# Kernel optimization log

Hardware: AMD Instinct MI355X
Metric: run time of the kernel (lower is better)

## Reference

```python
import jax, jax.numpy as jnp
import numpy as np

N, E, H, C, NG = 50000, 800000, 4, 64, 32
HC = H * C  # 256


def setup_inputs() -> dict:
    key = jax.random.key(0)
    ks = jax.random.split(key, 32)
    f32 = jnp.float32
    def rn(k, shape, s=0.1):
        return jax.random.normal(k, shape, dtype=f32) * s
    inp = {}
    inp['x'] = jax.random.normal(ks[0], (N, 4), dtype=f32)
    inp['edge_index'] = jax.random.randint(ks[1], (2, E), 0, N, dtype=jnp.int32)
    inp['edge_attr'] = jax.random.normal(ks[2], (E, 1), dtype=f32)
    inp['batch'] = jnp.sort(jax.random.randint(ks[3], (N,), 0, NG, dtype=jnp.int32))
    # encoder
    inp['enc_w'] = rn(ks[4], (4, 64)); inp['enc_b'] = rn(ks[5], (64,))
    # GATv2 layer 1: in 64 -> H*C (lin_l source, lin_r target, lin_edge, att, bias)
    inp['g1_wl'] = rn(ks[6], (64, HC)); inp['g1_bl'] = rn(ks[7], (HC,))
    inp['g1_wr'] = rn(ks[8], (64, HC)); inp['g1_br'] = rn(ks[9], (HC,))
    inp['g1_we'] = rn(ks[10], (1, HC))
    inp['g1_att'] = rn(ks[11], (H, C))
    inp['g1_bias'] = rn(ks[12], (HC,))
    # GATv2 layer 2: in 256 -> H*C
    inp['g2_wl'] = rn(ks[13], (HC, HC)); inp['g2_bl'] = rn(ks[14], (HC,))
    inp['g2_wr'] = rn(ks[15], (HC, HC)); inp['g2_br'] = rn(ks[16], (HC,))
    inp['g2_we'] = rn(ks[17], (1, HC))
    inp['g2_att'] = rn(ks[18], (H, C))
    inp['g2_bias'] = rn(ks[19], (HC,))
    # post MLP: 256 -> 128 (LayerNorm, ReLU) -> 64 (ReLU)
    inp['p1_w'] = rn(ks[20], (HC, 128)); inp['p1_b'] = rn(ks[21], (128,))
    inp['ln_g'] = jnp.ones((128,), dtype=f32); inp['ln_b'] = jnp.zeros((128,), dtype=f32)
    inp['p2_w'] = rn(ks[22], (128, 64)); inp['p2_b'] = rn(ks[23], (64,))
    return inp


def _gatv2_layer(x, src, dst, eattr, wl, bl, wr, br, we, att, bias):
    # PyG GATv2Conv: alpha_e = att . leaky_relu(lin_l(x_src) + lin_r(x_dst) + lin_edge(e))
    n = x.shape[0]
    xl = (x @ wl + bl).reshape(n, H, C)   # source-side messages
    xr = (x @ wr + br).reshape(n, H, C)   # target-side
    e = (eattr @ we).reshape(-1, H, C)
    m = jax.nn.leaky_relu(xl[src] + xr[dst] + e, 0.2)        # [E',H,C]
    alpha = jnp.einsum('ehc,hc->eh', m, att)                  # [E',H]
    amax = jax.lax.stop_gradient(jax.ops.segment_max(alpha, dst, num_segments=n))
    ex = jnp.exp(alpha - amax[dst])
    den = jax.ops.segment_sum(ex, dst, num_segments=n)
    a = ex / den[dst]                                          # softmax per dst node
    out = jax.ops.segment_sum(a[:, :, None] * xl[src], dst, num_segments=n)
    return out.reshape(n, HC) + bias


def reference(x, edge_index, edge_attr, batch, enc_w, enc_b,
              g1_wl, g1_bl, g1_wr, g1_br, g1_we, g1_att, g1_bias,
              g2_wl, g2_bl, g2_wr, g2_br, g2_we, g2_att, g2_bias,
              p1_w, p1_b, ln_g, ln_b, p2_w, p2_b):
    n = x.shape[0]
    src0, dst0 = edge_index[0], edge_index[1]
    # PyG default add_self_loops=True with fill_value='mean' for edge_attr
    deg = jnp.maximum(jax.ops.segment_sum(jnp.ones_like(edge_attr[:, 0]), dst0, num_segments=n), 1.0)
    loop_attr = jax.ops.segment_sum(edge_attr, dst0, num_segments=n) / deg[:, None]
    idx = jnp.arange(n, dtype=src0.dtype)
    src = jnp.concatenate([src0, idx]); dst = jnp.concatenate([dst0, idx])
    eattr = jnp.concatenate([edge_attr, loop_attr], axis=0)
    h = jax.nn.relu(x @ enc_w + enc_b)
    h = jax.nn.relu(_gatv2_layer(h, src, dst, eattr, g1_wl, g1_bl, g1_wr, g1_br, g1_we, g1_att, g1_bias))
    h = jax.nn.relu(_gatv2_layer(h, src, dst, eattr, g2_wl, g2_bl, g2_wr, g2_br, g2_we, g2_att, g2_bias))
    # global mean pool over graphs
    cnt = jnp.maximum(jax.ops.segment_sum(jnp.ones((n,), h.dtype), batch, num_segments=NG), 1.0)
    g = jax.ops.segment_sum(h, batch, num_segments=NG) / cnt[:, None]
    # post MLP (dropout is identity in eval)
    z = g @ p1_w + p1_b
    mu = jnp.mean(z, axis=-1, keepdims=True)
    var = jnp.mean((z - mu) ** 2, axis=-1, keepdims=True)
    z = (z - mu) / jnp.sqrt(var + 1e-5) * ln_g + ln_b
    z = jax.nn.relu(z)
    z = jax.nn.relu(z @ p2_w + p2_b)
    return z
```

## Files before the change

### kernel.cpp

```cpp
#include <hip/hip_runtime.h>

#define CDIV(a,b) (((a)+(b)-1)/(b))

typedef __bf16 bf16_t;
typedef bf16_t bf16x8 __attribute__((ext_vector_type(8)));
typedef bf16_t bf16x4 __attribute__((ext_vector_type(4)));
typedef float floatx4 __attribute__((ext_vector_type(4)));
typedef float floatx2 __attribute__((ext_vector_type(2)));

__device__ __forceinline__ int sigma2(int p) {
    int tile = p >> 7, hh = (p >> 6) & 1, m = (p >> 2) & 15, c = p & 3;
    return tile * 128 + (hh * 4 + c) * 16 + m;
}

__device__ __forceinline__ floatx2 up2(unsigned v) {
    floatx2 r;
    r.x = __uint_as_float(v << 16);
    r.y = __uint_as_float(v & 0xffff0000u);
    return r;
}

__global__ void k_deg(const int* __restrict__ ei, const float* __restrict__ ea,
                      float* __restrict__ deg, float* __restrict__ lsum, int E) {
    int e = blockIdx.x * 256 + threadIdx.x;
    if (e >= E) return;
    int d = ei[E + e];
    atomicAdd(&deg[d], 1.0f);
    atomicAdd(&lsum[d], ea[e]);
}

__global__ void k_loopattr(float* __restrict__ lsum, const float* __restrict__ deg, int n) {
    int i = blockIdx.x * 256 + threadIdx.x;
    if (i >= n) return;
    lsum[i] = lsum[i] / fmaxf(deg[i], 1.0f);
}

__global__ void k_scanA(const float* __restrict__ deg, int* __restrict__ part, int n) {
    __shared__ int sh[256];
    int t = threadIdx.x;
    int i = blockIdx.x * 256 + t;
    int v = (i < n) ? (int)deg[i] + 1 : 0;
    sh[t] = v;
    __syncthreads();
    for (int d = 128; d > 0; d >>= 1) { if (t < d) sh[t] += sh[t + d]; __syncthreads(); }
    if (t == 0) part[blockIdx.x] = sh[0];
}
__global__ void k_scanB(int* __restrict__ part, int nb) {
    __shared__ int sh[256];
    int t = threadIdx.x;
    int v = (t < nb) ? part[t] : 0;
    sh[t] = v;
    __syncthreads();
    for (int d = 1; d < 256; d <<= 1) {
        int u = (t >= d) ? sh[t - d] : 0;
        __syncthreads();
        sh[t] += u;
        __syncthreads();
    }
    if (t < nb) part[t] = sh[t] - v;
}
__global__ void k_scanC(const float* __restrict__ deg, const int* __restrict__ part,
                        int* __restrict__ off, int n) {
    __shared__ int sh[256];
    int t = threadIdx.x;
    int i = blockIdx.x * 256 + t;
    int v = (i < n) ? (int)deg[i] + 1 : 0;
    sh[t] = v;
    __syncthreads();
    for (int d = 1; d < 256; d <<= 1) {
        int u = (t >= d) ? sh[t - d] : 0;
        __syncthreads();
        sh[t] += u;
        __syncthreads();
    }
    int excl = part[blockIdx.x] + sh[t] - v;
    if (i < n) off[i] = excl;
    if (i == n - 1) off[n] = excl + v;
}

__global__ void k_fill(const int* __restrict__ ei, const float* __restrict__ ea,
                       const float* __restrict__ lattr, const int* __restrict__ off,
                       int* __restrict__ cursor, int* __restrict__ csr_src,
                       float* __restrict__ csr_ea, int E, int n) {
    int e = blockIdx.x * 256 + threadIdx.x;
    int EE = E + n;
    if (e >= EE) return;
    int s, d; float a;
    if (e < E) { s = ei[e]; d = ei[E + e]; a = ea[e]; }
    else       { s = e - E; d = s;         a = lattr[s]; }
    int pos = off[d] + atomicAdd(&cursor[d], 1);
    csr_src[pos] = s;
    csr_ea[pos] = a;
}

__global__ void k_enc(const float* __restrict__ x, const float* __restrict__ w,
                      const float* __restrict__ b, bf16_t* __restrict__ h0, int n) {
    int idx = blockIdx.x * 256 + threadIdx.x;
    if (idx >= n * 64) return;
    int nn = idx >> 6, j = idx & 63;
    const float* xr = x + (size_t)nn * 4;
    float s = b[j];
#pragma unroll
    for (int k = 0; k < 4; ++k) s = fmaf(xr[k], w[k * 64 + j], s);
    h0[idx] = (bf16_t)fmaxf(s, 0.0f);
}

__global__ void k_wcast2(const float* __restrict__ Wl, const float* __restrict__ Wr,
                         const float* __restrict__ bl, const float* __restrict__ br,
                         bf16_t* __restrict__ Wt, float* __restrict__ bias2,
                         int K, int kshift, int permK,
                         const float* __restrict__ we, const float* __restrict__ att,
                         const float* __restrict__ cb,
                         float* __restrict__ wep, float* __restrict__ attp,
                         float* __restrict__ cbp) {
    int idx = blockIdx.x * 256 + threadIdx.x;
    if (idx < 512) bias2[idx] = (idx < 256) ? bl[idx] : br[idx - 256];
    if (idx < 256) {
        int sg = sigma2(idx);
        wep[idx] = we[sg]; attp[idx] = att[sg]; cbp[idx] = cb[sg];
    }
    if (idx >= 512 * K) return;
    int nn = idx >> kshift, k = idx & (K - 1);
    int ks = permK ? sigma2(k) : k;
    float v = (nn < 256) ? Wl[ks * 256 + nn] : Wr[ks * 256 + (nn - 256)];
    Wt[idx] = (bf16_t)v;
}

__global__ __launch_bounds__(256) void k_gemm_mfma(
        const bf16_t* __restrict__ Hb, const bf16_t* __restrict__ Wt,
        const float* __restrict__ bias2, bf16_t* __restrict__ XL,
        bf16_t* __restrict__ XR, int nrows, int K) {
    __shared__ bf16_t As[128 * 32];
    __shared__ bf16_t Bs[128 * 32];
    int tid = threadIdx.x;
    int w = tid >> 6, lane = tid & 63;
    int quad = lane >> 4, m = lane & 15;
    int row0 = blockIdx.x * 128;
    int n0 = blockIdx.y * 128;
    floatx4 acc[2][8];
#pragma unroll
    for (int rt = 0; rt < 2; ++rt)
#pragma unroll
        for (int ct = 0; ct < 8; ++ct)
            acc[rt][ct] = (floatx4){0.f, 0.f, 0.f, 0.f};

    for (int k0 = 0; k0 < K; k0 += 32) {
        __syncthreads();
#pragma unroll
        for (int i = 0; i < 2; ++i) {
            int c = tid + i * 256;
            int r = c >> 2, kc = c & 3;
            int sw = (kc + (r >> 1)) & 3;
            int gr = row0 + r; if (gr >= nrows) gr = nrows - 1;
            bf16x8 v = *(const bf16x8*)&Hb[(size_t)gr * K + k0 + kc * 8];
            *(bf16x8*)&As[r * 32 + sw * 8] = v;
        }
#pragma unroll
        for (int i = 0; i < 2; ++i) {
            int c = tid + i * 256;
            int r = c >> 2, kc = c & 3;
            int sw = (kc + (r >> 1)) & 3;
            bf16x8 v = *(const bf16x8*)&Wt[(size_t)(n0 + r) * K + k0 + kc * 8];
            *(bf16x8*)&Bs[r * 32 + sw * 8] = v;
        }
        __syncthreads();
        bf16x8 af[2], bfr[8];
#pragma unroll
        for (int rt = 0; rt < 2; ++rt) {
            int ar = w * 32 + rt * 16 + m;
            af[rt] = *(bf16x8*)&As[ar * 32 + (((quad + (ar >> 1)) & 3) * 8)];
        }
#pragma unroll
        for (int ct = 0; ct < 8; ++ct) {
            int br = ct * 16 + m;
            bfr[ct] = *(bf16x8*)&Bs[br * 32 + (((quad + (br >> 1)) & 3) * 8)];
        }
#pragma unroll
        for (int ct = 0; ct < 8; ++ct) {
            acc[0][ct] = __builtin_amdgcn_mfma_f32_16x16x32_bf16(af[0], bfr[ct], acc[0][ct], 0, 0, 0);
            acc[1][ct] = __builtin_amdgcn_mfma_f32_16x16x32_bf16(af[1], bfr[ct], acc[1][ct], 0, 0, 0);
        }
    }
    int tile = (n0 >> 7) & 1;
    bf16_t* dst = (n0 < 256) ? XL : XR;
    float bv[8];
#pragma unroll
    for (int ct = 0; ct < 8; ++ct) bv[ct] = bias2[n0 + ct * 16 + m];
#pragma unroll
    for (int rt = 0; rt < 2; ++rt) {
#pragma unroll
        for (int i = 0; i < 4; ++i) {
            int row = row0 + w * 32 + rt * 16 + quad * 4 + i;
            if (row < nrows) {
                bf16x4 v0, v1;
#pragma unroll
                for (int ct = 0; ct < 4; ++ct) {
                    v0[ct] = (bf16_t)(acc[rt][ct][i] + bv[ct]);
                    v1[ct] = (bf16_t)(acc[rt][ct + 4][i] + bv[ct + 4]);
                }
                *(bf16x4*)&dst[(size_t)row * 256 + tile * 128 + m * 4] = v0;
                *(bf16x4*)&dst[(size_t)row * 256 + tile * 128 + 64 + m * 4] = v1;
            }
        }
    }
}

__device__ __forceinline__ void pair_step(
        int p, int p1, int half, int loff,
        const int* __restrict__ csr_src, const float* __restrict__ csr_ea,
        const bf16_t* __restrict__ XL,
        floatx2 xr01, floatx2 xr23, floatx2 xr45, floatx2 xr67,
        floatx2 wv01, floatx2 wv23, floatx2 wv45, floatx2 wv67,
        floatx2 av01, floatx2 av23, floatx2 av45, floatx2 av67,
        float& s, floatx2& a01, floatx2& a23, floatx2& a45, floatx2& a67) {
    int idx = p + half;
    bool valid = idx < p1;
    int idc = valid ? idx : p1 - 1;
    int src = csr_src[idc];
    float eav = csr_ea[idc];
    uint4 u = *(const uint4*)((const char*)XL + (size_t)src * 512 + loff);
    floatx2 x01 = up2(u.x), x23 = up2(u.y), x45 = up2(u.z), x67 = up2(u.w);
    floatx2 t01 = x01 + xr01 + eav * wv01;
    floatx2 t23 = x23 + xr23 + eav * wv23;
    floatx2 t45 = x45 + xr45 + eav * wv45;
    floatx2 t67 = x67 + xr67 + eav * wv67;
    t01 = __builtin_elementwise_max(t01, 0.2f * t01);
    t23 = __builtin_elementwise_max(t23, 0.2f * t23);
    t45 = __builtin_elementwise_max(t45, 0.2f * t45);
    t67 = __builtin_elementwise_max(t67, 0.2f * t67);
    floatx2 d = t01 * av01 + t23 * av23 + t45 * av45 + t67 * av67;
    float al = d.x + d.y;
    al += __shfl_xor(al, 1);
    al += __shfl_xor(al, 2);
    al += __shfl_xor(al, 4);
    float wg = valid ? exp2f(al) : 0.0f;
    s += wg;
    a01 += wg * x01; a23 += wg * x23; a45 += wg * x45; a67 += wg * x67;
}

__global__ void k_conv(const bf16_t* __restrict__ XL, const bf16_t* __restrict__ XR,
                       const float* __restrict__ wep, const float* __restrict__ attp,
                       const int* __restrict__ csr_src, const float* __restrict__ csr_ea,
                       const int* __restrict__ off, const float* __restrict__ cbp,
                       bf16_t* __restrict__ outb, int n) {
    int wid = (blockIdx.x * 256 + threadIdx.x) >> 6;
    int lane = threadIdx.x & 63;
    if (wid >= n) return;
    int l = lane & 31, half = lane >> 5;
    int loff = l * 16;
    uint4 ur = *(const uint4*)((const char*)XR + (size_t)wid * 512 + loff);
    floatx2 xr01 = up2(ur.x), xr23 = up2(ur.y), xr45 = up2(ur.z), xr67 = up2(ur.w);
    float4 wa = ((const float4*)wep)[2 * l], wb = ((const float4*)wep)[2 * l + 1];
    float4 aa = ((const float4*)attp)[2 * l], ab = ((const float4*)attp)[2 * l + 1];
    floatx2 wv01 = {wa.x, wa.y}, wv23 = {wa.z, wa.w};
    floatx2 wv45 = {wb.x, wb.y}, wv67 = {wb.z, wb.w};
    const float LOG2E = 1.44269504f;
    floatx2 av01 = {aa.x * LOG2E, aa.y * LOG2E}, av23 = {aa.z * LOG2E, aa.w * LOG2E};
    floatx2 av45 = {ab.x * LOG2E, ab.y * LOG2E}, av67 = {ab.z * LOG2E, ab.w * LOG2E};
    int p0 = off[wid], p1 = off[wid + 1];
    float s = 0.f;
    floatx2 a01 = {0.f, 0.f}, a23 = {0.f, 0.f}, a45 = {0.f, 0.f}, a67 = {0.f, 0.f};
    int p = p0;
    for (; p + 4 <= p1; p += 4) {
        pair_step(p,     p1, half, loff, csr_src, csr_ea, XL, xr01, xr23, xr45, xr67,
                  wv01, wv23, wv45, wv67, av01, av23, av45, av67, s, a01, a23, a45, a67);
        pair_step(p + 2, p1, half, loff, csr_src, csr_ea, XL, xr01, xr23, xr45, xr67,
                  wv01, wv23, wv45, wv67, av01, av23, av45, av67, s, a01, a23, a45, a67);
    }
    for (; p < p1; p += 2)
        pair_step(p,     p1, half, loff, csr_src, csr_ea, XL, xr01, xr23, xr45, xr67,
                  wv01, wv23, wv45, wv67, av01, av23, av45, av67, s, a01, a23, a45, a67);
    s += __shfl_xor(s, 32);
    a01.x += __shfl_xor(a01.x, 32); a01.y += __shfl_xor(a01.y, 32);
    a23.x += __shfl_xor(a23.x, 32); a23.y += __shfl_xor(a23.y, 32);
    a45.x += __shfl_xor(a45.x, 32); a45.y += __shfl_xor(a45.y, 32);
    a67.x += __shfl_xor(a67.x, 32); a67.y += __shfl_xor(a67.y, 32);
    if (half == 0) {
        float inv = 1.0f / s;
        float4 ba = ((const float4*)cbp)[2 * l], bb = ((const float4*)cbp)[2 * l + 1];
        bf16x8 ob;
        ob[0] = (bf16_t)fmaxf(fmaf(a01.x, inv, ba.x), 0.f);
        ob[1] = (bf16_t)fmaxf(fmaf(a01.y, inv, ba.y), 0.f);
        ob[2] = (bf16_t)fmaxf(fmaf(a23.x, inv, ba.z), 0.f);
        ob[3] = (bf16_t)fmaxf(fmaf(a23.y, inv, ba.w), 0.f);
        ob[4] = (bf16_t)fmaxf(fmaf(a45.x, inv, bb.x), 0.f);
        ob[5] = (bf16_t)fmaxf(fmaf(a45.y, inv, bb.y), 0.f);
        ob[6] = (bf16_t)fmaxf(fmaf(a67.x, inv, bb.z), 0.f);
        ob[7] = (bf16_t)fmaxf(fmaf(a67.y, inv, bb.w), 0.f);
        *(bf16x8*)&outb[(size_t)wid * 256 + l * 8] = ob;
    }
}

__global__ void k_pool(const bf16_t* __restrict__ h, const int* __restrict__ batch,
                       float* __restrict__ gsum, float* __restrict__ gcnt, int n) {
    int j = threadIdx.x;
    int start = blockIdx.x * 32;
    if (start >= n) return;
    int end = start + 32; if (end > n) end = n;
    int cur = batch[start];
    float acc = 0.0f, cnt = 0.0f;
    for (int i = start; i < end; ++i) {
        int g = batch[i];
        if (g != cur) {
            atomicAdd(&gsum[cur * 256 + j], acc);
            if (j == 0) atomicAdd(&gcnt[cur], cnt);
            acc = 0.0f; cnt = 0.0f; cur = g;
        }
        acc += (float)h[(size_t)i * 256 + j];
        cnt += 1.0f;
    }
    atomicAdd(&gsum[cur * 256 + j], acc);
    if (j == 0) atomicAdd(&gcnt[cur], cnt);
}

__global__ void k_mlp(const float* __restrict__ gsum, const float* __restrict__ gcnt,
                      const float* __restrict__ p1w, const float* __restrict__ p1b,
                      const float* __restrict__ lng, const float* __restrict__ lnb,
                      const float* __restrict__ p2w, const float* __restrict__ p2b,
                      float* __restrict__ out) {
    int g = blockIdx.x;
    int t = threadIdx.x;
    __shared__ float gv[256];
    __shared__ float z[128];
    __shared__ float red[128];
    float invc = 1.0f / fmaxf(gcnt[g], 1.0f);
    gv[sigma2(t)]       = gsum[g * 256 + t] * invc;
    gv[sigma2(t + 128)] = gsum[g * 256 + 128 + t] * invc;
    __syncthreads();
    float z1 = p1b[t];
    for (int k = 0; k < 256; ++k) z1 = fmaf(gv[k], p1w[k * 128 + t], z1);
    red[t] = z1;
    __syncthreads();
    for (int d = 64; d > 0; d >>= 1) { if (t < d) red[t] += red[t + d]; __syncthreads(); }
    float mu = red[0] * (1.0f / 128.0f);
    __syncthreads();
    float dz = z1 - mu;
    red[t] = dz * dz;
    __syncthreads();
    for (int d = 64; d > 0; d >>= 1) { if (t < d) red[t] += red[t + d]; __syncthreads(); }
    float var = red[0] * (1.0f / 128.0f);
    float zn = dz * rsqrtf(var + 1e-5f) * lng[t] + lnb[t];
    z[t] = fmaxf(zn, 0.0f);
    __syncthreads();
    if (t < 64) {
        float o = p2b[t];
        for (int k = 0; k < 128; ++k) o = fmaf(z[k], p2w[k * 64 + t], o);
        out[g * 64 + t] = fmaxf(o, 0.0f);
    }
}

extern "C" void kernel_launch(void* const* d_in, const int* in_sizes, int n_in,
                              void* d_out, int out_size, void* d_ws, size_t ws_size,
                              hipStream_t stream) {
    const float* x      = (const float*)d_in[0];
    const int*   ei     = (const int*)d_in[1];
    const float* ea     = (const float*)d_in[2];
    const int*   batch  = (const int*)d_in[3];
    const float* enc_w  = (const float*)d_in[4];
    const float* enc_b  = (const float*)d_in[5];
    const float* g1_wl  = (const float*)d_in[6];
    const float* g1_bl  = (const float*)d_in[7];
    const float* g1_wr  = (const float*)d_in[8];
    const float* g1_br  = (const float*)d_in[9];
    const float* g1_we  = (const float*)d_in[10];
    const float* g1_att = (const float*)d_in[11];
    const float* g1_bias= (const float*)d_in[12];
    const float* g2_wl  = (const float*)d_in[13];
    const float* g2_bl  = (const float*)d_in[14];
    const float* g2_wr  = (const float*)d_in[15];
    const float* g2_br  = (const float*)d_in[16];
    const float* g2_we  = (const float*)d_in[17];
    const float* g2_att = (const float*)d_in[18];
    const float* g2_bias= (const float*)d_in[19];
    const float* p1_w   = (const float*)d_in[20];
    const float* p1_b   = (const float*)d_in[21];
    const float* ln_g   = (const float*)d_in[22];
    const float* ln_b   = (const float*)d_in[23];
    const float* p2_w   = (const float*)d_in[24];
    const float* p2_b   = (const float*)d_in[25];
    float* out = (float*)d_out;

    const int N  = in_sizes[3];
    const int E  = in_sizes[1] / 2;
    const int EE = E + N;
    const int NB = CDIV(N, 256);

    bf16_t* XL  = (bf16_t*)d_ws;
    bf16_t* XR  = XL + (size_t)N * 256;
    bf16_t* Hb  = XR + (size_t)N * 256;
    bf16_t* Wt  = Hb + (size_t)N * 256;
    float* csr_ea= (float*)(Wt + 512 * 256);
    float* bias2 = csr_ea + EE;
    float* wep   = bias2 + 512;
    float* attp  = wep + 256;
    float* cbp   = attp + 256;
    float* deg   = cbp + 256;
    float* lsum  = deg + N;
    float* gsum  = lsum + N;
    float* gcnt  = gsum + 32 * 256;
    int*   cursor= (int*)(gcnt + 32);
    int*   part  = cursor + N;
    int*   off   = part + 256;
    int*   csr_src = off + (N + 1);

    hipMemsetAsync(deg, 0, (size_t)(3 * N + 32 * 256 + 32) * sizeof(float), stream);

    k_deg<<<CDIV(E, 256), 256, 0, stream>>>(ei, ea, deg, lsum, E);
    k_loopattr<<<CDIV(N, 256), 256, 0, stream>>>(lsum, deg, N);
    k_scanA<<<NB, 256, 0, stream>>>(deg, part, N);
    k_scanB<<<1, 256, 0, stream>>>(part, NB);
    k_scanC<<<NB, 256, 0, stream>>>(deg, part, off, N);
    k_fill<<<CDIV(EE, 256), 256, 0, stream>>>(ei, ea, lsum, off, cursor, csr_src, csr_ea, E, N);
    k_enc<<<CDIV(N * 64, 256), 256, 0, stream>>>(x, enc_w, enc_b, Hb, N);

    dim3 ggrid(CDIV(N, 128), 4);

    k_wcast2<<<CDIV(512 * 64, 256), 256, 0, stream>>>(g1_wl, g1_wr, g1_bl, g1_br, Wt, bias2,
                                                      64, 6, 0, g1_we, g1_att, g1_bias,
                                                      wep, attp, cbp);
    k_gemm_mfma<<<ggrid, 256, 0, stream>>>(Hb, Wt, bias2, XL, XR, N, 64);
    k_conv<<<CDIV(N, 4), 256, 0, stream>>>(XL, XR, wep, attp, csr_src, csr_ea, off, cbp, Hb, N);

    k_wcast2<<<CDIV(512 * 256, 256), 256, 0, stream>>>(g2_wl, g2_wr, g2_bl, g2_br, Wt, bias2,
                                                       256, 8, 1, g2_we, g2_att, g2_bias,
                                                       wep, attp, cbp);
    k_gemm_mfma<<<ggrid, 256, 0, stream>>>(Hb, Wt, bias2, XL, XR, N, 256);
    k_conv<<<CDIV(N, 4), 256, 0, stream>>>(XL, XR, wep, attp, csr_src, csr_ea, off, cbp, Hb, N);

    k_pool<<<CDIV(N, 32), 256, 0, stream>>>(Hb, batch, gsum, gcnt, N);
    k_mlp<<<32, 128, 0, stream>>>(gsum, gcnt, p1_w, p1_b, ln_g, ln_b, p2_w, p2_b, out);
}
```

Before: 512.2 us.

## Fuse encoder into first GEMM, pack CSR edges, drop loopattr kernel

Folds the node encoder (x@enc_w+b, ReLU) into the A-tile load of the first MFMA GEMM, so the separate encoder kernel and its bf16 activation round-trip go away. The loop-attr division is merged into the scan kernel, and the degree counter becomes an integer atomic. CSR source index and edge attribute are packed into one int2 array, so the conv kernel issues one 8-byte load per edge instead of two. The conv kernel also gets launch bounds with 8 blocks per SM. In exchange, the encoder is recomputed once per output-column tile (four times per row), and the occupancy bound may cause register spills.

```diff
diff --git a/kernel.cpp b/kernel.cpp
--- a/kernel.cpp
+++ b/kernel.cpp
@@ -21,25 +21,19 @@
 }
 
 __global__ void k_deg(const int* __restrict__ ei, const float* __restrict__ ea,
-                      float* __restrict__ deg, float* __restrict__ lsum, int E) {
+                      int* __restrict__ deg, float* __restrict__ lsum, int E) {
     int e = blockIdx.x * 256 + threadIdx.x;
     if (e >= E) return;
     int d = ei[E + e];
-    atomicAdd(&deg[d], 1.0f);
+    atomicAdd(&deg[d], 1);
     atomicAdd(&lsum[d], ea[e]);
 }
 
-__global__ void k_loopattr(float* __restrict__ lsum, const float* __restrict__ deg, int n) {
-    int i = blockIdx.x * 256 + threadIdx.x;
-    if (i >= n) return;
-    lsum[i] = lsum[i] / fmaxf(deg[i], 1.0f);
-}
-
-__global__ void k_scanA(const float* __restrict__ deg, int* __restrict__ part, int n) {
+__global__ void k_scanA(const int* __restrict__ deg, int* __restrict__ part, int n) {
     __shared__ int sh[256];
     int t = threadIdx.x;
     int i = blockIdx.x * 256 + t;
-    int v = (i < n) ? (int)deg[i] + 1 : 0;
+    int v = (i < n) ? deg[i] + 1 : 0;
     sh[t] = v;
     __syncthreads();
     for (int d = 128; d > 0; d >>= 1) { if (t < d) sh[t] += sh[t + d]; __syncthreads(); }
@@ -59,12 +53,13 @@
     }
     if (t < nb) part[t] = sh[t] - v;
 }
-__global__ void k_scanC(const float* __restrict__ deg, const int* __restrict__ part,
-                        int* __restrict__ off, int n) {
+__global__ void k_scanC(const int* __restrict__ deg, const int* __restrict__ part,
+                        int* __restrict__ off, float* __restrict__ lsum, int n) {
     __shared__ int sh[256];
     int t = threadIdx.x;
     int i = blockIdx.x * 256 + t;
-    int v = (i < n) ? (int)deg[i] + 1 : 0;
+    int dv = (i < n) ? deg[i] : 0;
+    int v = (i < n) ? dv + 1 : 0;
     sh[t] = v;
     __syncthreads();
     for (int d = 1; d < 256; d <<= 1) {
@@ -74,14 +69,16 @@
         __syncthreads();
     }
     int excl = part[blockIdx.x] + sh[t] - v;
-    if (i < n) off[i] = excl;
+    if (i < n) {
+        off[i] = excl;
+        lsum[i] = lsum[i] / fmaxf((float)dv, 1.0f);
+    }
     if (i == n - 1) off[n] = excl + v;
 }
 
 __global__ void k_fill(const int* __restrict__ ei, const float* __restrict__ ea,
                        const float* __restrict__ lattr, const int* __restrict__ off,
-                       int* __restrict__ cursor, int* __restrict__ csr_src,
-                       float* __restrict__ csr_ea, int E, int n) {
+                       int* __restrict__ cursor, int2* __restrict__ csr, int E, int n) {
     int e = blockIdx.x * 256 + threadIdx.x;
     int EE = E + n;
     if (e >= EE) return;
@@ -89,20 +86,7 @@
     if (e < E) { s = ei[e]; d = ei[E + e]; a = ea[e]; }
     else       { s = e - E; d = s;         a = lattr[s]; }
     int pos = off[d] + atomicAdd(&cursor[d], 1);
-    csr_src[pos] = s;
-    csr_ea[pos] = a;
-}
-
-__global__ void k_enc(const float* __restrict__ x, const float* __restrict__ w,
-                      const float* __restrict__ b, bf16_t* __restrict__ h0, int n) {
-    int idx = blockIdx.x * 256 + threadIdx.x;
-    if (idx >= n * 64) return;
-    int nn = idx >> 6, j = idx & 63;
-    const float* xr = x + (size_t)nn * 4;
-    float s = b[j];
-#pragma unroll
-    for (int k = 0; k < 4; ++k) s = fmaf(xr[k], w[k * 64 + j], s);
-    h0[idx] = (bf16_t)fmaxf(s, 0.0f);
+    csr[pos] = make_int2(s, __float_as_int(a));
 }
 
 __global__ void k_wcast2(const float* __restrict__ Wl, const float* __restrict__ Wr,
@@ -126,6 +110,97 @@
     Wt[idx] = (bf16_t)v;
 }
 
+__global__ __launch_bounds__(256) void k_gemm1_fused(
+        const float* __restrict__ x, const float* __restrict__ encw,
+        const float* __restrict__ encb, const bf16_t* __restrict__ Wt,
+        const float* __restrict__ bias2, bf16_t* __restrict__ XL,
+        bf16_t* __restrict__ XR, int nrows) {
+    __shared__ bf16_t As[128 * 32];
+    __shared__ bf16_t Bs[128 * 32];
+    int tid = threadIdx.x;
+    int w = tid >> 6, lane = tid & 63;
+    int quad = lane >> 4, m = lane & 15;
+    int row0 = blockIdx.x * 128;
+    int n0 = blockIdx.y * 128;
+    floatx4 acc[2][8];
+#pragma unroll
+    for (int rt = 0; rt < 2; ++rt)
+#pragma unroll
+        for (int ct = 0; ct < 8; ++ct)
+            acc[rt][ct] = (floatx4){0.f, 0.f, 0.f, 0.f};
+
+    for (int k0 = 0; k0 < 64; k0 += 32) {
+        __syncthreads();
+#pragma unroll
+        for (int i = 0; i < 2; ++i) {
+            int c = tid + i * 256;
+            int r = c >> 2, kc = c & 3;
+            int sw = (kc + (r >> 1)) & 3;
+            int gr = row0 + r; if (gr >= nrows) gr = nrows - 1;
+            float4 xv = ((const float4*)x)[gr];
+            bf16x8 v;
+#pragma unroll
+            for (int kk = 0; kk < 8; ++kk) {
+                int k = k0 + kc * 8 + kk;
+                float s = encb[k];
+                s = fmaf(xv.x, encw[k], s);
+                s = fmaf(xv.y, encw[64 + k], s);
+                s = fmaf(xv.z, encw[128 + k], s);
+                s = fmaf(xv.w, encw[192 + k], s);
+                v[kk] = (bf16_t)fmaxf(s, 0.0f);
+            }
+            *(bf16x8*)&As[r * 32 + sw * 8] = v;
+        }
+#pragma unroll
+        for (int i = 0; i < 2; ++i) {
+            int c = tid + i * 256;
+            int r = c >> 2, kc = c & 3;
+            int sw = (kc + (r >> 1)) & 3;
+            bf16x8 v = *(const bf16x8*)&Wt[(size_t)(n0 + r) * 64 + k0 + kc * 8];
+            *(bf16x8*)&Bs[r * 32 + sw * 8] = v;
+        }
+        __syncthreads();
+        bf16x8 af[2], bfr[8];
+#pragma unroll
+        for (int rt = 0; rt < 2; ++rt) {
+            int ar = w * 32 + rt * 16 + m;
+            af[rt] = *(bf16x8*)&As[ar * 32 + (((quad + (ar >> 1)) & 3) * 8)];
+        }
+#pragma unroll
+        for (int ct = 0; ct < 8; ++ct) {
+            int br = ct * 16 + m;
+            bfr[ct] = *(bf16x8*)&Bs[br * 32 + (((quad + (br >> 1)) & 3) * 8)];
+        }
+#pragma unroll
+        for (int ct = 0; ct < 8; ++ct) {
+            acc[0][ct] = __builtin_amdgcn_mfma_f32_16x16x32_bf16(af[0], bfr[ct], acc[0][ct], 0, 0, 0);
+            acc[1][ct] = __builtin_amdgcn_mfma_f32_16x16x32_bf16(af[1], bfr[ct], acc[1][ct], 0, 0, 0);
+        }
+    }
+    int tile = (n0 >> 7) & 1;
+    bf16_t* dst = (n0 < 256) ? XL : XR;
+    float bv[8];
+#pragma unroll
+    for (int ct = 0; ct < 8; ++ct) bv[ct] = bias2[n0 + ct * 16 + m];
+#pragma unroll
+    for (int rt = 0; rt < 2; ++rt) {
+#pragma unroll
+        for (int i = 0; i < 4; ++i) {
+            int row = row0 + w * 32 + rt * 16 + quad * 4 + i;
+            if (row < nrows) {
+                bf16x4 v0, v1;
+#pragma unroll
+                for (int ct = 0; ct < 4; ++ct) {
+                    v0[ct] = (bf16_t)(acc[rt][ct][i] + bv[ct]);
+                    v1[ct] = (bf16_t)(acc[rt][ct + 4][i] + bv[ct + 4]);
+                }
+                *(bf16x4*)&dst[(size_t)row * 256 + tile * 128 + m * 4] = v0;
+                *(bf16x4*)&dst[(size_t)row * 256 + tile * 128 + 64 + m * 4] = v1;
+            }
+        }
+    }
+}
+
 __global__ __launch_bounds__(256) void k_gemm_mfma(
         const bf16_t* __restrict__ Hb, const bf16_t* __restrict__ Wt,
         const float* __restrict__ bias2, bf16_t* __restrict__ XL,
@@ -207,8 +282,7 @@
 
 __device__ __forceinline__ void pair_step(
         int p, int p1, int half, int loff,
-        const int* __restrict__ csr_src, const float* __restrict__ csr_ea,
-        const bf16_t* __restrict__ XL,
+        const int2* __restrict__ csr, const bf16_t* __restrict__ XL,
         floatx2 xr01, floatx2 xr23, floatx2 xr45, floatx2 xr67,
         floatx2 wv01, floatx2 wv23, floatx2 wv45, floatx2 wv67,
         floatx2 av01, floatx2 av23, floatx2 av45, floatx2 av67,
@@ -216,8 +290,9 @@
     int idx = p + half;
     bool valid = idx < p1;
     int idc = valid ? idx : p1 - 1;
-    int src = csr_src[idc];
-    float eav = csr_ea[idc];
+    int2 ed = csr[idc];
+    int src = ed.x;
+    float eav = __int_as_float(ed.y);
     uint4 u = *(const uint4*)((const char*)XL + (size_t)src * 512 + loff);
     floatx2 x01 = up2(u.x), x23 = up2(u.y), x45 = up2(u.z), x67 = up2(u.w);
     floatx2 t01 = x01 + xr01 + eav * wv01;
@@ -238,9 +313,10 @@
     a01 += wg * x01; a23 += wg * x23; a45 += wg * x45; a67 += wg * x67;
 }
 
-__global__ void k_conv(const bf16_t* __restrict__ XL, const bf16_t* __restrict__ XR,
+__global__ __launch_bounds__(256, 8) void k_conv(
+                       const bf16_t* __restrict__ XL, const bf16_t* __restrict__ XR,
                        const float* __restrict__ wep, const float* __restrict__ attp,
-                       const int* __restrict__ csr_src, const float* __restrict__ csr_ea,
+                       const int2* __restrict__ csr,
                        const int* __restrict__ off, const float* __restrict__ cbp,
                        bf16_t* __restrict__ outb, int n) {
     int wid = (blockIdx.x * 256 + threadIdx.x) >> 6;
@@ -262,13 +338,13 @@
     floatx2 a01 = {0.f, 0.f}, a23 = {0.f, 0.f}, a45 = {0.f, 0.f}, a67 = {0.f, 0.f};
     int p = p0;
     for (; p + 4 <= p1; p += 4) {
-        pair_step(p,     p1, half, loff, csr_src, csr_ea, XL, xr01, xr23, xr45, xr67,
+        pair_step(p,     p1, half, loff, csr, XL, xr01, xr23, xr45, xr67,
                   wv01, wv23, wv45, wv67, av01, av23, av45, av67, s, a01, a23, a45, a67);
-        pair_step(p + 2, p1, half, loff, csr_src, csr_ea, XL, xr01, xr23, xr45, xr67,
+        pair_step(p + 2, p1, half, loff, csr, XL, xr01, xr23, xr45, xr67,
                   wv01, wv23, wv45, wv67, av01, av23, av45, av67, s, a01, a23, a45, a67);
     }
     for (; p < p1; p += 2)
-        pair_step(p,     p1, half, loff, csr_src, csr_ea, XL, xr01, xr23, xr45, xr67,
+        pair_step(p,     p1, half, loff, csr, XL, xr01, xr23, xr45, xr67,
                   wv01, wv23, wv45, wv67, av01, av23, av45, av67, s, a01, a23, a45, a67);
     s += __shfl_xor(s, 32);
     a01.x += __shfl_xor(a01.x, 32); a01.y += __shfl_xor(a01.y, 32);
@@ -389,43 +465,40 @@
     bf16_t* XR  = XL + (size_t)N * 256;
     bf16_t* Hb  = XR + (size_t)N * 256;
     bf16_t* Wt  = Hb + (size_t)N * 256;
-    float* csr_ea= (float*)(Wt + 512 * 256);
-    float* bias2 = csr_ea + EE;
+    int2*  csr  = (int2*)(Wt + 512 * 256);
+    float* lsum  = (float*)(csr + EE);
+    float* gsum  = lsum + N;
+    float* gcnt  = gsum + 32 * 256;
+    int*   deg   = (int*)(gcnt + 32);
+    int*   cursor= deg + N;
+    float* bias2 = (float*)(cursor + N);
     float* wep   = bias2 + 512;
     float* attp  = wep + 256;
     float* cbp   = attp + 256;
-    float* deg   = cbp + 256;
-    float* lsum  = deg + N;
-    float* gsum  = lsum + N;
-    float* gcnt  = gsum + 32 * 256;
-    int*   cursor= (int*)(gcnt + 32);
-    int*   part  = cursor + N;
+    int*   part  = (int*)(cbp + 256);
     int*   off   = part + 256;
-    int*   csr_src = off + (N + 1);
-
-    hipMemsetAsync(deg, 0, (size_t)(3 * N + 32 * 256 + 32) * sizeof(float), stream);
+
+    hipMemsetAsync(lsum, 0, (size_t)(3 * N + 32 * 256 + 32) * sizeof(float), stream);
 
     k_deg<<<CDIV(E, 256), 256, 0, stream>>>(ei, ea, deg, lsum, E);
-    k_loopattr<<<CDIV(N, 256), 256, 0, stream>>>(lsum, deg, N);
     k_scanA<<<NB, 256, 0, stream>>>(deg, part, N);
     k_scanB<<<1, 256, 0, stream>>>(part, NB);
-    k_scanC<<<NB, 256, 0, stream>>>(deg, part, off, N);
-    k_fill<<<CDIV(EE, 256), 256, 0, stream>>>(ei, ea, lsum, off, cursor, csr_src, csr_ea, E, N);
-    k_enc<<<CDIV(N * 64, 256), 256, 0, stream>>>(x, enc_w, enc_b, Hb, N);
+    k_scanC<<<NB, 256, 0, stream>>>(deg, part, off, lsum, N);
+    k_fill<<<CDIV(EE, 256), 256, 0, stream>>>(ei, ea, lsum, off, cursor, csr, E, N);
 
     dim3 ggrid(CDIV(N, 128), 4);
 
     k_wcast2<<<CDIV(512 * 64, 256), 256, 0, stream>>>(g1_wl, g1_wr, g1_bl, g1_br, Wt, bias2,
                                                       64, 6, 0, g1_we, g1_att, g1_bias,
                                                       wep, attp, cbp);
-    k_gemm_mfma<<<ggrid, 256, 0, stream>>>(Hb, Wt, bias2, XL, XR, N, 64);
-    k_conv<<<CDIV(N, 4), 256, 0, stream>>>(XL, XR, wep, attp, csr_src, csr_ea, off, cbp, Hb, N);
+    k_gemm1_fused<<<ggrid, 256, 0, stream>>>(x, enc_w, enc_b, Wt, bias2, XL, XR, N);
+    k_conv<<<CDIV(N, 4), 256, 0, stream>>>(XL, XR, wep, attp, csr, off, cbp, Hb, N);
 
     k_wcast2<<<CDIV(512 * 256, 256), 256, 0, stream>>>(g2_wl, g2_wr, g2_bl, g2_br, Wt, bias2,
                                                        256, 8, 1, g2_we, g2_att, g2_bias,
                                                        wep, attp, cbp);
     k_gemm_mfma<<<ggrid, 256, 0, stream>>>(Hb, Wt, bias2, XL, XR, N, 256);
-    k_conv<<<CDIV(N, 4), 256, 0, stream>>>(XL, XR, wep, attp, csr_src, csr_ea, off, cbp, Hb, N);
+    k_conv<<<CDIV(N, 4), 256, 0, stream>>>(XL, XR, wep, attp, csr, off, cbp, Hb, N);
 
     k_pool<<<CDIV(N, 32), 256, 0, stream>>>(Hb, batch, gsum, gcnt, N);
     k_mlp<<<32, 128, 0, stream>>>(gsum, gcnt, p1_w, p1_b, ln_g, ln_b, p2_w, p2_b, out);
```

Result: no change. 502.5 us (-1.9%).
